# Kernel tuning notes

Measured on AMD Instinct MI355X. Metric: run time of the kernel, lower is better.

Reference implementation:

```python
import jax, jax.numpy as jnp
import numpy as np

N_NODES = 40000
N_EDGES = 640000
IN_CH = 128
HID_CH = 256
EDGE_DIM = 64
N_SAMP = 2048
T = 1.0
EPS_GIN = 0.0
EPS_NORM = 1e-12


def setup_inputs() -> dict:
    key = jax.random.key(0)
    ks = jax.random.split(key, 12)
    x = jax.random.normal(ks[0], (N_NODES, IN_CH), dtype=jnp.float32)
    edge_index = jax.random.randint(ks[1], (2, N_EDGES), 0, N_NODES, dtype=jnp.int64)
    edge_attr = jax.random.normal(ks[2], (N_EDGES, EDGE_DIM), dtype=jnp.float32)
    pos_ind = jax.random.randint(ks[3], (N_SAMP,), 0, N_NODES, dtype=jnp.int64)
    neg_ind = jax.random.randint(ks[4], (N_SAMP,), 0, N_NODES, dtype=jnp.int64)
    # GINEConv internal edge projection Linear(64 -> 128)
    We = jax.random.normal(ks[5], (EDGE_DIM, IN_CH), dtype=jnp.float32) / np.sqrt(EDGE_DIM)
    be = jnp.zeros((IN_CH,), dtype=jnp.float32)
    # MLP: Linear(128->256), ReLU, Linear(256->256)
    W1 = jax.random.normal(ks[6], (IN_CH, HID_CH), dtype=jnp.float32) / np.sqrt(IN_CH)
    b1 = jnp.zeros((HID_CH,), dtype=jnp.float32)
    W2 = jax.random.normal(ks[7], (HID_CH, HID_CH), dtype=jnp.float32) / np.sqrt(HID_CH)
    b2 = jnp.zeros((HID_CH,), dtype=jnp.float32)
    thresholding_node = jax.random.normal(ks[8], (1, HID_CH), dtype=jnp.float32)
    return {"x": x, "edge_index": edge_index, "edge_attr": edge_attr,
            "pos_ind": pos_ind, "neg_ind": neg_ind,
            "We": We, "be": be, "W1": W1, "b1": b1, "W2": W2, "b2": b2,
            "thresholding_node": thresholding_node}


def _normalize(v):
    n = jnp.linalg.norm(v, axis=-1, keepdims=True)
    return v / jnp.maximum(n, EPS_NORM)


def reference(x, edge_index, edge_attr, pos_ind, neg_ind,
              We, be, W1, b1, W2, b2, thresholding_node):
    src, dst = edge_index[0], edge_index[1]  # PyG: message from x_j (src) to target i (dst)
    edge_emb = edge_attr @ We + be                    # [E, in_ch]
    msg = jax.nn.relu(x[src] + edge_emb)              # gather + add + relu
    agg = jax.ops.segment_sum(msg, dst, num_segments=x.shape[0])  # scatter-add
    h = (1.0 + EPS_GIN) * x + agg
    emb = jax.nn.relu(h @ W1 + b1) @ W2 + b2          # [N, hid]

    center = _normalize(emb[0])                       # [hid]
    pos = _normalize(emb[pos_ind])                    # [P, hid]
    neg = _normalize(emb[neg_ind])                    # [Q, hid]
    thr = _normalize(thresholding_node)               # [1, hid]

    pos_score_mean = (center[None, :] * pos).sum(-1).mean(-1)
    neg_score_mean = (center[None, :] * neg).sum(-1).mean(-1)
    thr_score = (center * thr).sum(-1)                # [1]

    pos_loss = jnp.log(jnp.clip(jax.nn.sigmoid((pos_score_mean - thr_score) / T), 1e-12)).mean()
    neg_loss = jnp.log(jnp.clip(jax.nn.sigmoid((thr_score - neg_score_mean) / T), 1e-12)).mean()
    return -pos_loss - neg_loss
```

## Files before the change

### kernel.cpp

```cpp
#include <hip/hip_runtime.h>
#include <math.h>

#define N_NODES 40000
#define N_EDGES 640000
#define IN_CH 128
#define HID_CH 256
#define EDGE_DIM 64
#define N_SAMP 2048
#define NSEL (1 + 2 * N_SAMP)
#define MAXU 4097

__global__ __launch_bounds__(256) void flag_kernel(
    const int* __restrict__ pos, const int* __restrict__ neg,
    int* __restrict__ slot, int* __restrict__ counters)
{
    int r = blockIdx.x * 256 + threadIdx.x;
    if (r >= NSEL) return;
    int node = (r == 0) ? 0 : (r <= N_SAMP ? pos[r - 1] : neg[r - 1 - N_SAMP]);
    int old = atomicCAS(&slot[node], -1, -2);
    if (old == -1) slot[node] = atomicAdd(&counters[1], 1);
}

__global__ __launch_bounds__(256) void compact_kernel(
    const int* __restrict__ ei, const int* __restrict__ slot,
    int* __restrict__ counters, int* __restrict__ eid,
    int* __restrict__ esrc, int* __restrict__ eslot)
{
    const int tid = threadIdx.x, wave = tid >> 6, lane = tid & 63;
    const int e = blockIdx.x * 256 + tid;
    const int d = ei[N_EDGES + e];
    const int sl = slot[d];
    const bool valid = (sl >= 0);
    unsigned long long m = __ballot(valid);
    int wrank = __popcll(m & ((1ULL << lane) - 1ULL));
    __shared__ int woff[4];
    __shared__ int bbase;
    if (lane == 0) woff[wave] = __popcll(m);
    __syncthreads();
    if (tid == 0) {
        int t = 0;
        for (int i = 0; i < 4; ++i) { int c = woff[i]; woff[i] = t; t += c; }
        bbase = atomicAdd(&counters[0], t);
    }
    __syncthreads();
    if (valid) {
        int idx = bbase + woff[wave] + wrank;
        eid[idx] = e;
        esrc[idx] = ei[e];
        eslot[idx] = sl;
    }
}

__global__ __launch_bounds__(256) void edge_kernel(
    const float* __restrict__ x, const float* __restrict__ edge_attr,
    const float* __restrict__ We, const float* __restrict__ be,
    const int* __restrict__ counters, const int* __restrict__ eid,
    const int* __restrict__ esrc, const int* __restrict__ eslot,
    float* __restrict__ agg_c)
{
    __shared__ float sWe[EDGE_DIM * IN_CH];
    __shared__ float sAttr[4][16 * EDGE_DIM];
    __shared__ int sE[4][16], sS[4][16], sL[4][16];
    const int tid = threadIdx.x, wave = tid >> 6, lane = tid & 63;
    const int M = counters[0];

    {
        const float4* s4 = (const float4*)We;
        float4* d4 = (float4*)sWe;
        for (int i = tid; i < (EDGE_DIM * IN_CH) / 4; i += 256) d4[i] = s4[i];
    }
    __syncthreads();
    const float be0 = be[lane], be1 = be[64 + lane];

    for (int b = blockIdx.x * 64; b < M; b += gridDim.x * 64) {
        const int wb = b + wave * 16;
        if (lane < 16) {
            int idx = wb + lane;
            bool v = idx < M;
            int ic = v ? idx : 0;
            sE[wave][lane] = eid[ic];
            sS[wave][lane] = esrc[ic];
            sL[wave][lane] = v ? eslot[ic] : -1;
        }
        __syncthreads();
        {
            int sub = lane >> 4, q = lane & 15;
#pragma unroll
            for (int p = 0; p < 4; ++p) {
                int j = p * 4 + sub;
                int e = sE[wave][j];
                ((float4*)&sAttr[wave][j * EDGE_DIM])[q] =
                    ((const float4*)(edge_attr + (size_t)e * EDGE_DIM))[q];
            }
        }
        __syncthreads();

        float acc0[16], acc1[16];
#pragma unroll
        for (int j = 0; j < 16; ++j) { acc0[j] = 0.f; acc1[j] = 0.f; }
        for (int k0 = 0; k0 < EDGE_DIM; k0 += 4) {
            float w0[4], w1[4];
#pragma unroll
            for (int kk = 0; kk < 4; ++kk) {
                w0[kk] = sWe[(k0 + kk) * IN_CH + lane];
                w1[kk] = sWe[(k0 + kk) * IN_CH + 64 + lane];
            }
#pragma unroll
            for (int j = 0; j < 16; ++j) {
                float4 a = *(const float4*)&sAttr[wave][j * EDGE_DIM + k0];
                acc0[j] += a.x * w0[0] + a.y * w0[1] + a.z * w0[2] + a.w * w0[3];
                acc1[j] += a.x * w1[0] + a.y * w1[1] + a.z * w1[2] + a.w * w1[3];
            }
        }
        for (int j = 0; j < 16; ++j) {
            int sl = sL[wave][j];
            if (sl < 0) continue;
            int s = sS[wave][j];
            float m0 = fmaxf(x[(size_t)s * IN_CH + lane] + acc0[j] + be0, 0.f);
            float m1 = fmaxf(x[(size_t)s * IN_CH + 64 + lane] + acc1[j] + be1, 0.f);
            atomicAdd(&agg_c[(size_t)sl * IN_CH + lane], m0);
            atomicAdd(&agg_c[(size_t)sl * IN_CH + 64 + lane], m1);
        }
        __syncthreads();
    }
}

__global__ __launch_bounds__(256) void mlp1_kernel(
    const float* __restrict__ x, const float* __restrict__ agg_c,
    const int* __restrict__ slot, const int* __restrict__ pos,
    const int* __restrict__ neg, const float* __restrict__ W1,
    const float* __restrict__ b1, float* __restrict__ hid)
{
    __shared__ float sh[16][IN_CH];
    __shared__ int snode[16], sslot[16];
    const int tid = threadIdx.x;
    const int r0 = blockIdx.x * 16;
    if (tid < 16) {
        int r = r0 + tid;
        int node = 0;
        if (r < NSEL && r > 0) node = (r <= N_SAMP) ? pos[r - 1] : neg[r - 1 - N_SAMP];
        snode[tid] = node;
        sslot[tid] = slot[node];
    }
    __syncthreads();
    for (int i = tid; i < 16 * (IN_CH / 4); i += 256) {
        int rr = i >> 5, k4 = i & 31;
        int n = snode[rr], sl = sslot[rr];
        float4 xa = ((const float4*)(x + (size_t)n * IN_CH))[k4];
        float4 ga = ((const float4*)(agg_c + (size_t)sl * IN_CH))[k4];
        ((float4*)sh[rr])[k4] =
            make_float4(xa.x + ga.x, xa.y + ga.y, xa.z + ga.z, xa.w + ga.w);
    }
    __syncthreads();
    float acc[16];
#pragma unroll
    for (int rr = 0; rr < 16; ++rr) acc[rr] = 0.f;
#pragma unroll 4
    for (int k = 0; k < IN_CH; ++k) {
        float w = W1[k * HID_CH + tid];
#pragma unroll
        for (int rr = 0; rr < 16; ++rr) acc[rr] += sh[rr][k] * w;
    }
    float bb = b1[tid];
#pragma unroll
    for (int rr = 0; rr < 16; ++rr) {
        int r = r0 + rr;
        if (r < NSEL) hid[(size_t)r * HID_CH + tid] = fmaxf(acc[rr] + bb, 0.f);
    }
}

__global__ __launch_bounds__(256) void mlp2_kernel(
    const float* __restrict__ hid, const float* __restrict__ W2,
    const float* __restrict__ b2, float* __restrict__ emb)
{
    __shared__ float sh[16][HID_CH];
    const int tid = threadIdx.x;
    const int r0 = blockIdx.x * 16;
    for (int i = tid; i < 16 * (HID_CH / 4); i += 256) {
        int rr = i >> 6, k4 = i & 63;
        int r = r0 + rr;
        float4 v = (r < NSEL) ? ((const float4*)(hid + (size_t)r * HID_CH))[k4]
                              : make_float4(0.f, 0.f, 0.f, 0.f);
        ((float4*)sh[rr])[k4] = v;
    }
    __syncthreads();
    float acc[16];
#pragma unroll
    for (int rr = 0; rr < 16; ++rr) acc[rr] = 0.f;
#pragma unroll 4
    for (int k = 0; k < HID_CH; ++k) {
        float w = W2[k * HID_CH + tid];
#pragma unroll
        for (int rr = 0; rr < 16; ++rr) acc[rr] += sh[rr][k] * w;
    }
    float bb = b2[tid];
#pragma unroll
    for (int rr = 0; rr < 16; ++rr) {
        int r = r0 + rr;
        if (r < NSEL) emb[(size_t)r * HID_CH + tid] = acc[rr] + bb;
    }
}

__global__ __launch_bounds__(256) void score_kernel(
    const float* __restrict__ emb, float* __restrict__ partial)
{
    const int tid = threadIdx.x;
    const int wave = tid >> 6, lane = tid & 63;
    const int rid = blockIdx.x * 4 + wave;
    const float4 c = ((const float4*)emb)[lane];
    const float4 v = ((const float4*)(emb + (size_t)(rid + 1) * HID_CH))[lane];
    float cc = c.x * c.x + c.y * c.y + c.z * c.z + c.w * c.w;
    float vv = v.x * v.x + v.y * v.y + v.z * v.z + v.w * v.w;
    float cv = c.x * v.x + c.y * v.y + c.z * v.z + c.w * v.w;
#pragma unroll
    for (int off = 32; off; off >>= 1) {
        cc += __shfl_xor(cc, off, 64);
        vv += __shfl_xor(vv, off, 64);
        cv += __shfl_xor(cv, off, 64);
    }
    float score = cv / (fmaxf(sqrtf(cc), 1e-12f) * fmaxf(sqrtf(vv), 1e-12f));
    __shared__ float wsum[4];
    if (lane == 0) wsum[wave] = score;
    __syncthreads();
    if (tid == 0) partial[blockIdx.x] = wsum[0] + wsum[1] + wsum[2] + wsum[3];
}

__global__ __launch_bounds__(64) void loss_kernel(
    const float* __restrict__ emb, const float* __restrict__ thrn,
    const float* __restrict__ partial, float* __restrict__ out)
{
    const int lane = threadIdx.x;
    const float4 c = ((const float4*)emb)[lane];
    const float4 t = ((const float4*)thrn)[lane];
    float cc = c.x * c.x + c.y * c.y + c.z * c.z + c.w * c.w;
    float tt = t.x * t.x + t.y * t.y + t.z * t.z + t.w * t.w;
    float ct = c.x * t.x + c.y * t.y + c.z * t.z + c.w * t.w;
    float ps = 0.f, ns = 0.f;
#pragma unroll
    for (int i = 0; i < 8; ++i) ps += partial[lane + 64 * i];
#pragma unroll
    for (int i = 0; i < 8; ++i) ns += partial[512 + lane + 64 * i];
#pragma unroll
    for (int off = 32; off; off >>= 1) {
        cc += __shfl_xor(cc, off, 64);
        tt += __shfl_xor(tt, off, 64);
        ct += __shfl_xor(ct, off, 64);
        ps += __shfl_xor(ps, off, 64);
        ns += __shfl_xor(ns, off, 64);
    }
    if (lane == 0) {
        float thr = ct / (fmaxf(sqrtf(cc), 1e-12f) * fmaxf(sqrtf(tt), 1e-12f));
        float pm = ps / (float)N_SAMP;
        float nm = ns / (float)N_SAMP;
        float s1 = 1.f / (1.f + expf(-(pm - thr)));
        float s2 = 1.f / (1.f + expf(-(thr - nm)));
        s1 = fmaxf(s1, 1e-12f);
        s2 = fmaxf(s2, 1e-12f);
        out[0] = -(logf(s1) + logf(s2));
    }
}

extern "C" void kernel_launch(void* const* d_in, const int* in_sizes, int n_in,
                              void* d_out, int out_size, void* d_ws, size_t ws_size,
                              hipStream_t stream)
{
    const float* x         = (const float*)d_in[0];
    const int*   ei        = (const int*)d_in[1];
    const float* edge_attr = (const float*)d_in[2];
    const int*   pos       = (const int*)d_in[3];
    const int*   neg       = (const int*)d_in[4];
    const float* We        = (const float*)d_in[5];
    const float* be        = (const float*)d_in[6];
    const float* W1        = (const float*)d_in[7];
    const float* b1        = (const float*)d_in[8];
    const float* W2        = (const float*)d_in[9];
    const float* b2        = (const float*)d_in[10];
    const float* thrn      = (const float*)d_in[11];
    float* out = (float*)d_out;

    int* slot     = (int*)d_ws;
    int* counters = slot + 40960;
    int* eid      = counters + 32;
    int* esrc     = eid + N_EDGES;
    int* eslot    = esrc + N_EDGES;
    float* agg_c  = (float*)(eslot + N_EDGES);
    float* hid    = agg_c + 524800;
    float* emb    = hid + 1048832;
    float* partial= emb + 1048832;

    hipMemsetAsync(slot, 0xFF, 40960 * sizeof(int), stream);
    hipMemsetAsync(counters, 0, 32 * sizeof(int), stream);
    hipMemsetAsync(agg_c, 0, (size_t)MAXU * IN_CH * sizeof(float), stream);

    flag_kernel<<<(NSEL + 255) / 256, 256, 0, stream>>>(pos, neg, slot, counters);
    compact_kernel<<<N_EDGES / 256, 256, 0, stream>>>(ei, slot, counters, eid, esrc, eslot);
    edge_kernel<<<1024, 256, 0, stream>>>(x, edge_attr, We, be, counters, eid, esrc, eslot, agg_c);
    mlp1_kernel<<<(NSEL + 15) / 16, 256, 0, stream>>>(x, agg_c, slot, pos, neg, W1, b1, hid);
    mlp2_kernel<<<(NSEL + 15) / 16, 256, 0, stream>>>(hid, W2, b2, emb);
    score_kernel<<<1024, 256, 0, stream>>>(emb, partial);
    loss_kernel<<<1, 64, 0, stream>>>(emb, thrn, partial, out);
}
```

Baseline: 369.9 us.

## Sort compacted edges by destination slot and fuse MLP layers

Adds a histogram, scan and scatter pass that groups the compacted edges by destination slot. The edge kernel can then sum consecutive messages to the same slot in registers and issue fewer atomics. The three memsets become a single init kernel, the edge metadata is packed into int4 records, and the two MLP kernels are fused so the hidden activations stay in shared memory. In exchange it adds two extra launches and an atomic scatter pass, and since the graph is random only about 6 edges share each slot, so few get merged within a 16-edge batch.

```diff
diff --git a/kernel.cpp b/kernel.cpp
--- a/kernel.cpp
+++ b/kernel.cpp
@@ -9,6 +9,20 @@
 #define N_SAMP 2048
 #define NSEL (1 + 2 * N_SAMP)
 #define MAXU 4097
+#define HBUCKETS 5120
+
+__global__ __launch_bounds__(256) void init_kernel(
+    int* __restrict__ slot, int* __restrict__ counters,
+    int* __restrict__ hist, float4* __restrict__ agg4)
+{
+    const int i = blockIdx.x * 256 + threadIdx.x;
+    const int n = gridDim.x * 256;
+    for (int j = i; j < 40960; j += n) slot[j] = -1;
+    for (int j = i; j < HBUCKETS; j += n) hist[j] = 0;
+    for (int j = i; j < 32; j += n) counters[j] = 0;
+    const float4 z = make_float4(0.f, 0.f, 0.f, 0.f);
+    for (int j = i; j < (MAXU * IN_CH) / 4; j += n) agg4[j] = z;
+}
 
 __global__ __launch_bounds__(256) void flag_kernel(
     const int* __restrict__ pos, const int* __restrict__ neg,
@@ -23,8 +37,7 @@
 
 __global__ __launch_bounds__(256) void compact_kernel(
     const int* __restrict__ ei, const int* __restrict__ slot,
-    int* __restrict__ counters, int* __restrict__ eid,
-    int* __restrict__ esrc, int* __restrict__ eslot)
+    int* __restrict__ counters, int* __restrict__ hist, int4* __restrict__ cmp)
 {
     const int tid = threadIdx.x, wave = tid >> 6, lane = tid & 63;
     const int e = blockIdx.x * 256 + tid;
@@ -45,17 +58,48 @@
     __syncthreads();
     if (valid) {
         int idx = bbase + woff[wave] + wrank;
-        eid[idx] = e;
-        esrc[idx] = ei[e];
-        eslot[idx] = sl;
+        cmp[idx] = make_int4(e, ei[e], sl, 0);
+        atomicAdd(&hist[sl], 1);
+    }
+}
+
+__global__ __launch_bounds__(1024) void scan_kernel(
+    const int* __restrict__ hist, int* __restrict__ cursor)
+{
+    __shared__ int tmp[1024];
+    const int t = threadIdx.x;
+    int v[5]; int s = 0;
+#pragma unroll
+    for (int i = 0; i < 5; ++i) { v[i] = hist[t * 5 + i]; s += v[i]; }
+    tmp[t] = s;
+    __syncthreads();
+    for (int d = 1; d < 1024; d <<= 1) {
+        int a = (t >= d) ? tmp[t - d] : 0;
+        __syncthreads();
+        tmp[t] += a;
+        __syncthreads();
+    }
+    int run = tmp[t] - s;
+#pragma unroll
+    for (int i = 0; i < 5; ++i) { cursor[t * 5 + i] = run; run += v[i]; }
+}
+
+__global__ __launch_bounds__(256) void scatter_kernel(
+    const int4* __restrict__ cmp, const int* __restrict__ counters,
+    int* __restrict__ cursor, int4* __restrict__ sorted)
+{
+    const int M = counters[0];
+    for (int i = blockIdx.x * 256 + threadIdx.x; i < M; i += gridDim.x * 256) {
+        int4 c = cmp[i];
+        int p = atomicAdd(&cursor[c.z], 1);
+        sorted[p] = c;
     }
 }
 
 __global__ __launch_bounds__(256) void edge_kernel(
     const float* __restrict__ x, const float* __restrict__ edge_attr,
     const float* __restrict__ We, const float* __restrict__ be,
-    const int* __restrict__ counters, const int* __restrict__ eid,
-    const int* __restrict__ esrc, const int* __restrict__ eslot,
+    const int* __restrict__ counters, const int4* __restrict__ sorted,
     float* __restrict__ agg_c)
 {
     __shared__ float sWe[EDGE_DIM * IN_CH];
@@ -77,10 +121,10 @@
         if (lane < 16) {
             int idx = wb + lane;
             bool v = idx < M;
-            int ic = v ? idx : 0;
-            sE[wave][lane] = eid[ic];
-            sS[wave][lane] = esrc[ic];
-            sL[wave][lane] = v ? eslot[ic] : -1;
+            int4 c = sorted[v ? idx : 0];
+            sE[wave][lane] = c.x;
+            sS[wave][lane] = c.y;
+            sL[wave][lane] = v ? c.z : -1;
         }
         __syncthreads();
         {
@@ -112,26 +156,39 @@
                 acc1[j] += a.x * w1[0] + a.y * w1[1] + a.z * w1[2] + a.w * w1[3];
             }
         }
+
+        float sum0 = 0.f, sum1 = 0.f;
+#pragma unroll
         for (int j = 0; j < 16; ++j) {
             int sl = sL[wave][j];
-            if (sl < 0) continue;
-            int s = sS[wave][j];
-            float m0 = fmaxf(x[(size_t)s * IN_CH + lane] + acc0[j] + be0, 0.f);
-            float m1 = fmaxf(x[(size_t)s * IN_CH + 64 + lane] + acc1[j] + be1, 0.f);
-            atomicAdd(&agg_c[(size_t)sl * IN_CH + lane], m0);
-            atomicAdd(&agg_c[(size_t)sl * IN_CH + 64 + lane], m1);
-        }
-        __syncthreads();
-    }
-}
-
-__global__ __launch_bounds__(256) void mlp1_kernel(
+            if (sl >= 0) {
+                int s = sS[wave][j];
+                float m0 = fmaxf(x[(size_t)s * IN_CH + lane] + acc0[j] + be0, 0.f);
+                float m1 = fmaxf(x[(size_t)s * IN_CH + 64 + lane] + acc1[j] + be1, 0.f);
+                sum0 += m0;
+                sum1 += m1;
+                bool flush = (j == 15) || (sL[wave][j + 1] != sl);
+                if (flush) {
+                    atomicAdd(&agg_c[(size_t)sl * IN_CH + lane], sum0);
+                    atomicAdd(&agg_c[(size_t)sl * IN_CH + 64 + lane], sum1);
+                    sum0 = 0.f;
+                    sum1 = 0.f;
+                }
+            }
+        }
+        __syncthreads();
+    }
+}
+
+__global__ __launch_bounds__(256) void mlp_kernel(
     const float* __restrict__ x, const float* __restrict__ agg_c,
     const int* __restrict__ slot, const int* __restrict__ pos,
     const int* __restrict__ neg, const float* __restrict__ W1,
-    const float* __restrict__ b1, float* __restrict__ hid)
-{
-    __shared__ float sh[16][IN_CH];
+    const float* __restrict__ b1, const float* __restrict__ W2,
+    const float* __restrict__ b2, float* __restrict__ emb)
+{
+    __shared__ float sin_[16][IN_CH];
+    __shared__ float shid[16][HID_CH];
     __shared__ int snode[16], sslot[16];
     const int tid = threadIdx.x;
     const int r0 = blockIdx.x * 16;
@@ -148,56 +205,46 @@
         int n = snode[rr], sl = sslot[rr];
         float4 xa = ((const float4*)(x + (size_t)n * IN_CH))[k4];
         float4 ga = ((const float4*)(agg_c + (size_t)sl * IN_CH))[k4];
-        ((float4*)sh[rr])[k4] =
+        ((float4*)sin_[rr])[k4] =
             make_float4(xa.x + ga.x, xa.y + ga.y, xa.z + ga.z, xa.w + ga.w);
     }
     __syncthreads();
+
     float acc[16];
 #pragma unroll
     for (int rr = 0; rr < 16; ++rr) acc[rr] = 0.f;
-#pragma unroll 4
-    for (int k = 0; k < IN_CH; ++k) {
-        float w = W1[k * HID_CH + tid];
-#pragma unroll
-        for (int rr = 0; rr < 16; ++rr) acc[rr] += sh[rr][k] * w;
-    }
-    float bb = b1[tid];
+    for (int k0 = 0; k0 < IN_CH; k0 += 4) {
+        float w[4];
+#pragma unroll
+        for (int kk = 0; kk < 4; ++kk) w[kk] = W1[(k0 + kk) * HID_CH + tid];
+#pragma unroll
+        for (int rr = 0; rr < 16; ++rr) {
+            float4 h = *(const float4*)&sin_[rr][k0];
+            acc[rr] += h.x * w[0] + h.y * w[1] + h.z * w[2] + h.w * w[3];
+        }
+    }
+    float bb1 = b1[tid];
+#pragma unroll
+    for (int rr = 0; rr < 16; ++rr) shid[rr][tid] = fmaxf(acc[rr] + bb1, 0.f);
+    __syncthreads();
+
+#pragma unroll
+    for (int rr = 0; rr < 16; ++rr) acc[rr] = 0.f;
+    for (int k0 = 0; k0 < HID_CH; k0 += 4) {
+        float w[4];
+#pragma unroll
+        for (int kk = 0; kk < 4; ++kk) w[kk] = W2[(k0 + kk) * HID_CH + tid];
+#pragma unroll
+        for (int rr = 0; rr < 16; ++rr) {
+            float4 h = *(const float4*)&shid[rr][k0];
+            acc[rr] += h.x * w[0] + h.y * w[1] + h.z * w[2] + h.w * w[3];
+        }
+    }
+    float bb2 = b2[tid];
 #pragma unroll
     for (int rr = 0; rr < 16; ++rr) {
         int r = r0 + rr;
-        if (r < NSEL) hid[(size_t)r * HID_CH + tid] = fmaxf(acc[rr] + bb, 0.f);
-    }
-}
-
-__global__ __launch_bounds__(256) void mlp2_kernel(
-    const float* __restrict__ hid, const float* __restrict__ W2,
-    const float* __restrict__ b2, float* __restrict__ emb)
-{
-    __shared__ float sh[16][HID_CH];
-    const int tid = threadIdx.x;
-    const int r0 = blockIdx.x * 16;
-    for (int i = tid; i < 16 * (HID_CH / 4); i += 256) {
-        int rr = i >> 6, k4 = i & 63;
-        int r = r0 + rr;
-        float4 v = (r < NSEL) ? ((const float4*)(hid + (size_t)r * HID_CH))[k4]
-                              : make_float4(0.f, 0.f, 0.f, 0.f);
-        ((float4*)sh[rr])[k4] = v;
-    }
-    __syncthreads();
-    float acc[16];
-#pragma unroll
-    for (int rr = 0; rr < 16; ++rr) acc[rr] = 0.f;
-#pragma unroll 4
-    for (int k = 0; k < HID_CH; ++k) {
-        float w = W2[k * HID_CH + tid];
-#pragma unroll
-        for (int rr = 0; rr < 16; ++rr) acc[rr] += sh[rr][k] * w;
-    }
-    float bb = b2[tid];
-#pragma unroll
-    for (int rr = 0; rr < 16; ++rr) {
-        int r = r0 + rr;
-        if (r < NSEL) emb[(size_t)r * HID_CH + tid] = acc[rr] + bb;
+        if (r < NSEL) emb[(size_t)r * HID_CH + tid] = acc[rr] + bb2;
     }
 }
 
@@ -280,23 +327,22 @@
 
     int* slot     = (int*)d_ws;
     int* counters = slot + 40960;
-    int* eid      = counters + 32;
-    int* esrc     = eid + N_EDGES;
-    int* eslot    = esrc + N_EDGES;
-    float* agg_c  = (float*)(eslot + N_EDGES);
-    float* hid    = agg_c + 524800;
-    float* emb    = hid + 1048832;
+    int* hist     = counters + 32;
+    int* cursor   = hist + HBUCKETS;
+    int4* cmp     = (int4*)(cursor + HBUCKETS);
+    int4* sorted  = cmp + N_EDGES;
+    float* agg_c  = (float*)(sorted + N_EDGES);
+    float* emb    = agg_c + 524800;
     float* partial= emb + 1048832;
 
-    hipMemsetAsync(slot, 0xFF, 40960 * sizeof(int), stream);
-    hipMemsetAsync(counters, 0, 32 * sizeof(int), stream);
-    hipMemsetAsync(agg_c, 0, (size_t)MAXU * IN_CH * sizeof(float), stream);
-
+    init_kernel<<<512, 256, 0, stream>>>(slot, counters, hist, (float4*)agg_c);
     flag_kernel<<<(NSEL + 255) / 256, 256, 0, stream>>>(pos, neg, slot, counters);
-    compact_kernel<<<N_EDGES / 256, 256, 0, stream>>>(ei, slot, counters, eid, esrc, eslot);
-    edge_kernel<<<1024, 256, 0, stream>>>(x, edge_attr, We, be, counters, eid, esrc, eslot, agg_c);
-    mlp1_kernel<<<(NSEL + 15) / 16, 256, 0, stream>>>(x, agg_c, slot, pos, neg, W1, b1, hid);
-    mlp2_kernel<<<(NSEL + 15) / 16, 256, 0, stream>>>(hid, W2, b2, emb);
+    compact_kernel<<<N_EDGES / 256, 256, 0, stream>>>(ei, slot, counters, hist, cmp);
+    scan_kernel<<<1, 1024, 0, stream>>>(hist, cursor);
+    scatter_kernel<<<256, 256, 0, stream>>>(cmp, counters, cursor, sorted);
+    edge_kernel<<<1024, 256, 0, stream>>>(x, edge_attr, We, be, counters, sorted, agg_c);
+    mlp_kernel<<<(NSEL + 15) / 16, 256, 0, stream>>>(x, agg_c, slot, pos, neg,
+                                                     W1, b1, W2, b2, emb);
     score_kernel<<<1024, 256, 0, stream>>>(emb, partial);
     loss_kernel<<<1, 64, 0, stream>>>(emb, thrn, partial, out);
 }
```

After: 367.4 us. Within noise of the previous version (-0.7%).
